# Performance work log

Hardware: AMD Instinct MI355X
Metric: run time of the kernel (lower is better)

The kernel has to match this reference:

```python
import jax, jax.numpy as jnp
import numpy as np

D = 1024   # dim == seq_len L (forced by final proj on [L, L])
N = 16     # SSM state size
K = 3      # conv kernel size, padding=1 -> same length


def setup_inputs() -> dict:
    key = jax.random.key(0)
    ks = jax.random.split(key, 8)
    s = lambda k, shape, sc: (jax.random.normal(k, shape, jnp.float32) * sc)
    return {
        "x": s(ks[0], (2, D, D), 1.0),
        "W_proj": s(ks[1], (D, D), D ** -0.5),
        "b_proj": jnp.zeros((D,), jnp.float32),
        "conv_w": s(ks[2], (D, D, K), (D * K) ** -0.5),  # [out_ch, in_ch, K]
        "conv_b": jnp.zeros((D,), jnp.float32),
        "A_log": jnp.log(jnp.tile(jnp.arange(1, N + 1, dtype=jnp.float32)[None, :], (D, 1))),  # [D, N]
        "W_delta": s(ks[3], (D, D), D ** -0.5),
        "W_B": s(ks[4], (D, N), D ** -0.5),
        "W_C": s(ks[5], (D, N), D ** -0.5),
    }


def _ssm(x, A_log, W_delta, W_B, W_C):
    # Mamba S6 diagonal selective scan. x: [L, D]
    delta = jax.nn.softplus(x @ W_delta)            # [L, D]
    B = x @ W_B                                      # [L, N]
    C = x @ W_C                                      # [L, N]
    A = -jnp.exp(A_log)                              # [D, N]
    Abar = jnp.exp(delta[:, :, None] * A[None])      # [L, D, N]
    Bx = (delta * x)[:, :, None] * B[:, None, :]     # [L, D, N]

    def combine(e1, e2):
        a1, b1 = e1
        a2, b2 = e2
        return a1 * a2, a2 * b1 + b2

    _, h = jax.lax.associative_scan(combine, (Abar, Bx), axis=0)  # h: [L, D, N]
    return jnp.einsum('ldn,ln->ld', h, C)            # [L, D]


def reference(x, W_proj, b_proj, conv_w, conv_b, A_log, W_delta, W_B, W_C):
    p = x @ W_proj.T + b_proj                        # shared proj; [2, L, D]
    xm, xg = p[0], p[1]                              # mirrors `x, x_ = self.proj(x)` unpacking batch==2
    xg = jax.nn.silu(xg)                             # [L, D]
    # Conv1d treats xm as (channels=L, length=D), padding=1 -> same length
    xc = jax.lax.conv_general_dilated(
        xm[None], conv_w, window_strides=(1,), padding=[(1, 1)],
        dimension_numbers=('NCW', 'OIW', 'NCW'))[0] + conv_b[:, None]  # [L, D]
    xc = jax.nn.silu(xc)
    y = _ssm(xc, A_log, W_delta, W_B, W_C)           # [L, D]
    y = y @ xg.T                                     # [L, L]  (x @ x_.transpose(-1,-2))
    return y @ W_proj.T + b_proj                     # final shared proj; [L, L]
```

## Files before the change

### kernel.cpp

```cpp
#include <hip/hip_runtime.h>
#include <math.h>


#define LL 1024
#define DD 1024
#define NS 16
#define CCH 16
#define CLEN 64

typedef short     bf16x8_t __attribute__((ext_vector_type(8)));
typedef float     f32x4_t  __attribute__((ext_vector_type(4)));
typedef unsigned short u16x4_t __attribute__((ext_vector_type(4)));
typedef unsigned short u16x8_t __attribute__((ext_vector_type(8)));

__device__ __forceinline__ float silu_f(float x) { return x / (1.f + expf(-x)); }
__device__ __forceinline__ float softplus_f(float x) {
  return fmaxf(x, 0.f) + log1pf(expf(-fabsf(x)));
}
__device__ __forceinline__ unsigned short f2bf(float f) {
  unsigned int u = __float_as_uint(f);
  u += 0x7fffu + ((u >> 16) & 1u);
  return (unsigned short)(u >> 16);
}

template<int N> __device__ __forceinline__ void s_wait_vmcnt() {
  asm volatile("s_waitcnt vmcnt(%0)" :: "n"(N) : "memory");
}
__device__ __forceinline__ void raw_barrier() {
  asm volatile("s_barrier" ::: "memory");
}

__global__ __launch_bounds__(256) void castk(const float* __restrict__ in,
                                             unsigned short* __restrict__ out, int n) {
  int i = (blockIdx.x * 256 + threadIdx.x) * 4;
  if (i >= n) return;
  float4 v = *(const float4*)(in + i);
  u16x4_t o; o[0] = f2bf(v.x); o[1] = f2bf(v.y); o[2] = f2bf(v.z); o[3] = f2bf(v.w);
  *(u16x4_t*)(out + i) = o;
}

__global__ __launch_bounds__(256) void tcastk(const float* __restrict__ W,
                                              unsigned short* __restrict__ out) {
  __shared__ float T[64][65];
  const int t = threadIdx.x;
  const int r = t >> 2, cq = (t & 3) << 4;
  const int d0 = blockIdx.x * 64, k0 = blockIdx.y * 64;
  #pragma unroll
  for (int c = 0; c < 16; c += 4) {
    float4 v = *(const float4*)&W[(size_t)(k0 + r) * DD + d0 + cq + c];
    T[r][cq + c + 0] = v.x; T[r][cq + c + 1] = v.y;
    T[r][cq + c + 2] = v.z; T[r][cq + c + 3] = v.w;
  }
  __syncthreads();
  u16x8_t o0, o1;
  #pragma unroll
  for (int j = 0; j < 8; ++j) o0[j] = f2bf(T[cq + j][r]);
  #pragma unroll
  for (int j = 0; j < 8; ++j) o1[j] = f2bf(T[cq + 8 + j][r]);
  *(u16x8_t*)&out[(size_t)(d0 + r) * DD + k0 + cq] = o0;
  *(u16x8_t*)&out[(size_t)(d0 + r) * DD + k0 + cq + 8] = o1;
}

__global__ __launch_bounds__(256) void bct_cast(const float* __restrict__ WB,
                                                const float* __restrict__ WC,
                                                unsigned short* __restrict__ wcomb) {
  const int b = blockIdx.x;
  const int k = threadIdx.x * 4;
  u16x4_t o;
  if (b < 32) {
    const float* W = (b < 16) ? WB : WC;
    const int n = b & 15;
    #pragma unroll
    for (int j = 0; j < 4; ++j) o[j] = f2bf(W[(size_t)(k + j) * NS + n]);
  } else {
    o[0] = o[1] = o[2] = o[3] = 0;
  }
  *(u16x4_t*)&wcomb[(size_t)(1024 + b) * DD + k] = o;
}

__global__ __launch_bounds__(256) void build_xsht(const unsigned short* __restrict__ xm,
                                                  unsigned short* __restrict__ out) {
  __shared__ unsigned short Xs[64][66];
  const int t = threadIdx.x;
  const int w0 = blockIdx.x * 64, i0 = blockIdx.y * 64;
  {
    const int r = t >> 2, cq = (t & 3) << 4;
    #pragma unroll
    for (int c = 0; c < 16; c += 4) {
      u16x4_t v = *(const u16x4_t*)&xm[(size_t)(i0 + r) * DD + w0 + cq + c];
      Xs[r][1 + cq + c + 0] = v[0]; Xs[r][1 + cq + c + 1] = v[1];
      Xs[r][1 + cq + c + 2] = v[2]; Xs[r][1 + cq + c + 3] = v[3];
    }
  }
  if (t < 64)                 Xs[t][0]       = (w0 > 0)        ? xm[(size_t)(i0 + t) * DD + w0 - 1]  : (unsigned short)0;
  else if (t < 128) { int r = t - 64; Xs[r][65] = (w0 + 64 < DD) ? xm[(size_t)(i0 + r) * DD + w0 + 64] : (unsigned short)0; }
  __syncthreads();
  const int wr = t >> 2, q = t & 3;
  unsigned short vals[48];
  #pragma unroll
  for (int ii = 0; ii < 16; ++ii)
    #pragma unroll
    for (int k = 0; k < 3; ++k)
      vals[ii * 3 + k] = Xs[q * 16 + ii][wr + k];
  #pragma unroll
  for (int s = 0; s < 6; ++s) {
    u16x8_t o;
    #pragma unroll
    for (int j = 0; j < 8; ++j) o[j] = vals[s * 8 + j];
    *(u16x8_t*)&out[(size_t)(w0 + wr) * 3072 + (size_t)i0 * 3 + q * 48 + s * 8] = o;
  }
}

__global__ __launch_bounds__(256) void gemm_sk(
    const unsigned short* __restrict__ A, const unsigned short* __restrict__ B,
    float* __restrict__ part, size_t sliceStride, int N, int K, int Ksl)
{
  constexpr int GI = 4;
  __shared__ unsigned short s[3][256 * 32];
  const int tid  = threadIdx.x;
  const int lane = tid & 63;
  const int wv   = tid >> 6;
  const int wm   = wv >> 1, wn = wv & 1;
  const int m0 = blockIdx.y * 128, n0 = blockIdx.x * 128;
  const int wbase = tid & 192;
  const int koff = blockIdx.z * Ksl;

  f32x4_t acc[4][4];
  #pragma unroll
  for (int i = 0; i < 4; ++i)
    #pragma unroll
    for (int j = 0; j < 4; ++j)
      acc[i][j] = (f32x4_t)(0.f);

  auto stage = [&](int buf, int kbase) {
    #pragma unroll
    for (int it = 0; it < GI; ++it) {
      const int c   = (it << 8) + tid;
      const int r   = c >> 2;
      const int kcg = (c & 3) ^ ((r >> 1) & 3);
      const unsigned short* src = (r < 128)
          ? (A + (size_t)(m0 + r) * K + kbase + kcg * 8)
          : (B + (size_t)(n0 + r - 128) * K + kbase + kcg * 8);
      __builtin_amdgcn_global_load_lds(
          (const __attribute__((address_space(1))) void*)src,
          (__attribute__((address_space(3))) void*)(&s[buf][0] + (size_t)((it << 8) + wbase) * 8),
          16, 0, 0);
    }
  };

  const int NT = Ksl >> 5;
  stage(0, koff);
  stage(1, koff + 32);
  s_wait_vmcnt<GI>();
  raw_barrier();

  for (int t = 0; t < NT; ++t) {
    if (t + 2 < NT) stage((t + 2) % 3, koff + (t + 2) * 32);

    const unsigned short* sb = &s[t % 3][0];
    const int rl = lane & 15, kq = lane >> 4;
    bf16x8_t af[4], bfr[4];
    #pragma unroll
    for (int mi = 0; mi < 4; ++mi) {
      const int row = wm * 64 + mi * 16 + rl;
      const int ch  = row * 4 + (kq ^ ((row >> 1) & 3));
      af[mi] = *(const bf16x8_t*)(sb + (size_t)ch * 8);
    }
    #pragma unroll
    for (int ni = 0; ni < 4; ++ni) {
      const int row = 128 + wn * 64 + ni * 16 + rl;
      const int ch  = row * 4 + (kq ^ ((row >> 1) & 3));
      bfr[ni] = *(const bf16x8_t*)(sb + (size_t)ch * 8);
    }
    #pragma unroll
    for (int mi = 0; mi < 4; ++mi)
      #pragma unroll
      for (int ni = 0; ni < 4; ++ni)
        acc[mi][ni] = __builtin_amdgcn_mfma_f32_16x16x32_bf16(af[mi], bfr[ni], acc[mi][ni], 0, 0, 0);

    if (t + 1 < NT) {
      if (t + 2 < NT) s_wait_vmcnt<GI>();
      else            s_wait_vmcnt<0>();
      raw_barrier();
    }
  }

  float* pz = part + (size_t)blockIdx.z * sliceStride;
  const int rl = lane & 15, rg = lane >> 4;
  #pragma unroll
  for (int mi = 0; mi < 4; ++mi) {
    #pragma unroll
    for (int ni = 0; ni < 4; ++ni) {
      const int col = n0 + wn * 64 + ni * 16 + rl;
      #pragma unroll
      for (int j = 0; j < 4; ++j) {
        const int row = m0 + wm * 64 + mi * 16 + rg * 4 + j;
        pz[(size_t)row * N + col] = acc[mi][ni][j];
      }
    }
  }
}

template<int SK, int ACT, bool O32, bool O16>
__global__ __launch_bounds__(256) void reduce_k(
    const float* __restrict__ part, size_t sliceStride,
    const float* __restrict__ bias,
    float* __restrict__ C32, unsigned short* __restrict__ C16)
{
  const size_t idx = ((size_t)blockIdx.x * 256 + threadIdx.x) * 4;
  const int row = (int)(idx >> 10), col = (int)(idx & 1023);
  float4 s = *(const float4*)&part[idx];
  #pragma unroll
  for (int z = 1; z < SK; ++z) {
    const float4 p = *(const float4*)&part[(size_t)z * sliceStride + idx];
    s.x += p.x; s.y += p.y; s.z += p.z; s.w += p.w;
  }
  float v[4] = {s.x, s.y, s.z, s.w};
  if (bias) {
    const float4 bv = *(const float4*)&bias[col];
    v[0] += bv.x; v[1] += bv.y; v[2] += bv.z; v[3] += bv.w;
  }
  #pragma unroll
  for (int j = 0; j < 4; ++j) {
    if (ACT == 2) v[j] = softplus_f(v[j]);
    else if (ACT == 3) { if (row >= 1024) v[j] = silu_f(v[j]); }
    else if (ACT == 4) { if (row < 1024)  v[j] = softplus_f(v[j]); }
  }
  if (O32) { float4 o; o.x = v[0]; o.y = v[1]; o.z = v[2]; o.w = v[3];
             *(float4*)&C32[idx] = o; }
  if (O16) { u16x4_t o; o[0] = f2bf(v[0]); o[1] = f2bf(v[1]);
             o[2] = f2bf(v[2]); o[3] = f2bf(v[3]);
             *(u16x4_t*)&C16[idx] = o; }
}

__global__ __launch_bounds__(256) void reduce_conv_t(
    const float* __restrict__ part, const float* __restrict__ cb,
    unsigned short* __restrict__ xc16, float* __restrict__ xcT)
{
  __shared__ float T[64][65];
  const int t = threadIdx.x;
  const int r = t >> 4;
  const int cq = (t & 15) << 2;
  const int r0 = blockIdx.y * 64, c0 = blockIdx.x * 64;
  #pragma unroll
  for (int rr = 0; rr < 64; rr += 16) {
    const int row = r0 + r + rr;
    const size_t base = (size_t)row * 1024 + c0 + cq;
    float4 s = *(const float4*)&part[base];
    #pragma unroll
    for (int z = 1; z < 4; ++z) {
      const float4 p = *(const float4*)&part[(size_t)z * (1024 * 1024) + base];
      s.x += p.x; s.y += p.y; s.z += p.z; s.w += p.w;
    }
    const float b = cb[row];
    float v[4] = {silu_f(s.x + b), silu_f(s.y + b), silu_f(s.z + b), silu_f(s.w + b)};
    u16x4_t o16; o16[0] = f2bf(v[0]); o16[1] = f2bf(v[1]);
    o16[2] = f2bf(v[2]); o16[3] = f2bf(v[3]);
    *(u16x4_t*)&xc16[base] = o16;
    T[r + rr][cq + 0] = v[0]; T[r + rr][cq + 1] = v[1];
    T[r + rr][cq + 2] = v[2]; T[r + rr][cq + 3] = v[3];
  }
  __syncthreads();
  #pragma unroll
  for (int rr = 0; rr < 64; rr += 16) {
    float4 o;
    o.x = T[cq + 0][r + rr]; o.y = T[cq + 1][r + rr];
    o.z = T[cq + 2][r + rr]; o.w = T[cq + 3][r + rr];
    *(float4*)&xcT[(size_t)(c0 + r + rr) * LL + r0 + cq] = o;
  }
}

__global__ __launch_bounds__(256) void scan_p1(
    const float* __restrict__ deltaT, const float* __restrict__ xcT,
    const float* __restrict__ BT, const float* __restrict__ A_log,
    float* __restrict__ P, float* __restrict__ H)
{
  const int tid = threadIdx.x;
  const int n = tid & 15, dl = tid >> 4;
  const int d = blockIdx.y * 16 + dl;
  const int c = blockIdx.x;
  const int l0 = c * CLEN;
  const float Av = -expf(A_log[d * NS + n]);
  float h = 0.f, p = 1.f;
  for (int j = 0; j < CLEN; j += 4) {
    const float4 dv = *(const float4*)&deltaT[(size_t)d * LL + l0 + j];
    const float4 xv = *(const float4*)&xcT[(size_t)d * LL + l0 + j];
    const float4 bv = *(const float4*)&BT[(size_t)n * LL + l0 + j];
    const float dvu[4] = {dv.x, dv.y, dv.z, dv.w};
    const float xvu[4] = {xv.x, xv.y, xv.z, xv.w};
    const float bvu[4] = {bv.x, bv.y, bv.z, bv.w};
    #pragma unroll
    for (int u = 0; u < 4; ++u) {
      const float ab = expf(dvu[u] * Av);
      h = fmaf(ab, h, dvu[u] * xvu[u] * bvu[u]);
      p *= ab;
    }
  }
  const int idx = d * NS + n;
  P[(size_t)c * (DD * NS) + idx] = p;
  H[(size_t)c * (DD * NS) + idx] = h;
}

__global__ __launch_bounds__(256) void scan_p2(const float* __restrict__ P,
                                               const float* __restrict__ H,
                                               float* __restrict__ Hin) {
  const int idx = blockIdx.x * 256 + threadIdx.x;
  float hin = 0.f;
  Hin[idx] = 0.f;
  #pragma unroll
  for (int c = 1; c < CCH; ++c) {
    hin = fmaf(P[(size_t)(c - 1) * (DD * NS) + idx], hin,
               H[(size_t)(c - 1) * (DD * NS) + idx]);
    Hin[(size_t)c * (DD * NS) + idx] = hin;
  }
}

__global__ __launch_bounds__(256) void scan_p3(
    const float* __restrict__ deltaT, const float* __restrict__ xcT,
    const float* __restrict__ BT, const float* __restrict__ CT,
    const float* __restrict__ Hin, const float* __restrict__ A_log,
    unsigned short* __restrict__ y16)
{
  const int tid = threadIdx.x;
  const int n = tid & 15, dl = tid >> 4;
  const int d = blockIdx.y * 16 + dl;
  const int c = blockIdx.x;
  const int l0 = c * CLEN;
  const float Av = -expf(A_log[d * NS + n]);
  float h = Hin[(size_t)c * (DD * NS) + d * NS + n];
  for (int j = 0; j < CLEN; j += 4) {
    const float4 dv = *(const float4*)&deltaT[(size_t)d * LL + l0 + j];
    const float4 xv = *(const float4*)&xcT[(size_t)d * LL + l0 + j];
    const float4 bv = *(const float4*)&BT[(size_t)n * LL + l0 + j];
    const float4 cv = *(const float4*)&CT[(size_t)n * LL + l0 + j];
    const float dvu[4] = {dv.x, dv.y, dv.z, dv.w};
    const float xvu[4] = {xv.x, xv.y, xv.z, xv.w};
    const float bvu[4] = {bv.x, bv.y, bv.z, bv.w};
    const float cvu[4] = {cv.x, cv.y, cv.z, cv.w};
    #pragma unroll
    for (int u = 0; u < 4; ++u) {
      const int l = l0 + j + u;
      const float ab = expf(dvu[u] * Av);
      h = fmaf(ab, h, dvu[u] * xvu[u] * bvu[u]);
      float contrib = h * cvu[u];
      contrib += __shfl_xor(contrib, 1);
      contrib += __shfl_xor(contrib, 2);
      contrib += __shfl_xor(contrib, 4);
      contrib += __shfl_xor(contrib, 8);
      if (n == 0) y16[(size_t)l * DD + d] = f2bf(contrib);
    }
  }
}

extern "C" void kernel_launch(void* const* d_in, const int* in_sizes, int n_in,
                              void* d_out, int out_size, void* d_ws, size_t ws_size,
                              hipStream_t stream) {
  const float* x       = (const float*)d_in[0];
  const float* W_proj  = (const float*)d_in[1];
  const float* b_proj  = (const float*)d_in[2];
  const float* conv_w  = (const float*)d_in[3];
  const float* conv_b  = (const float*)d_in[4];
  const float* A_log   = (const float*)d_in[5];
  const float* W_delta = (const float*)d_in[6];
  const float* W_B     = (const float*)d_in[7];
  const float* W_C     = (const float*)d_in[8];
  float* out = (float*)d_out;

  char* w = (char*)d_ws;
  const size_t QMB = 256 * 1024;
  unsigned short* wp16    = (unsigned short*)(w);
  unsigned short* pbuf    = (unsigned short*)(w + 8  * QMB);
  unsigned short* xm16    = pbuf;
  unsigned short* xg16    = pbuf + 1024 * 1024;
  unsigned short* wcomb16 = (unsigned short*)(w + 24 * QMB);
  unsigned short* xc16    = (unsigned short*)(w + 34 * QMB);
  float*          xcT32   = (float*)(w + 42 * QMB);
  unsigned short* x16     = (unsigned short*)(w + 58 * QMB);
  float*          dcomb32 = (float*)(w + 58 * QMB);
  float*          deltaT32= dcomb32;
  float*          BT32    = dcomb32 + (size_t)1024 * 1024;
  float*          CT32    = dcomb32 + (size_t)1040 * 1024;
  unsigned short* cw16    = (unsigned short*)(w + 75 * QMB);
  unsigned short* y16     = (unsigned short*)(w + 75 * QMB);
  float*          Pc      = (float*)(w + 83 * QMB);
  float*          Hc      = (float*)(w + 87 * QMB);
  float*          HinC    = (float*)(w + 91 * QMB);
  unsigned short* out116  = (unsigned short*)(w + 87 * QMB);
  unsigned short* xsht    = (unsigned short*)(w + 99 * QMB);
  float*          part    = (float*)(w + 123 * QMB);
  (void)ws_size;

  const dim3 blk(256);

  castk<<<dim3(2048), blk, 0, stream>>>(x, x16, 2 * 1024 * 1024);
  castk<<<dim3(1024), blk, 0, stream>>>(W_proj, wp16, 1024 * 1024);
  castk<<<dim3(3072), blk, 0, stream>>>(conv_w, cw16, 3 * 1024 * 1024);
  tcastk<<<dim3(16, 16), blk, 0, stream>>>(W_delta, wcomb16);
  bct_cast<<<dim3(128), blk, 0, stream>>>(W_B, W_C, wcomb16);

  gemm_sk<<<dim3(8, 16, 2), blk, 0, stream>>>(x16, wp16, part,
      (size_t)2048 * 1024, 1024, 1024, 512);
  reduce_k<2, 3, false, true><<<dim3(2048), blk, 0, stream>>>(
      part, (size_t)2048 * 1024, b_proj, nullptr, pbuf);
  build_xsht<<<dim3(16, 16), blk, 0, stream>>>(xm16, xsht);
  gemm_sk<<<dim3(8, 8, 4), blk, 0, stream>>>(cw16, xsht, part,
      (size_t)1024 * 1024, 1024, 3072, 768);
  reduce_conv_t<<<dim3(16, 16), blk, 0, stream>>>(part, conv_b, xc16, xcT32);
  gemm_sk<<<dim3(8, 9, 2), blk, 0, stream>>>(wcomb16, xc16, part,
      (size_t)1152 * 1024, 1024, 1024, 512);
  reduce_k<2, 4, true, false><<<dim3(1056), blk, 0, stream>>>(
      part, (size_t)1152 * 1024, nullptr, dcomb32, nullptr);
  scan_p1<<<dim3(CCH, DD / 16), blk, 0, stream>>>(deltaT32, xcT32, BT32, A_log, Pc, Hc);
  scan_p2<<<dim3(64), blk, 0, stream>>>(Pc, Hc, HinC);
  scan_p3<<<dim3(CCH, DD / 16), blk, 0, stream>>>(deltaT32, xcT32, BT32, CT32, HinC, A_log, y16);
  gemm_sk<<<dim3(8, 8, 4), blk, 0, stream>>>(y16, xg16, part,
      (size_t)1024 * 1024, 1024, 1024, 256);
  reduce_k<4, 0, false, true><<<dim3(1024), blk, 0, stream>>>(
      part, (size_t)1024 * 1024, nullptr, nullptr, out116);
  gemm_sk<<<dim3(8, 8, 4), blk, 0, stream>>>(out116, wp16, part,
      (size_t)1024 * 1024, 1024, 1024, 256);
  reduce_k<4, 0, true, false><<<dim3(1024), blk, 0, stream>>>(
      part, (size_t)1024 * 1024, b_proj, out, nullptr);
}
```

Before: 225.2 us.

## Shrink GEMM tiles to 64x64 with BK=64, fuse epilogue, cut split-K

The GEMM kernel now uses 64x64 output tiles with a 64-wide K step and an 8-way XOR swizzle, in place of 128x128 tiles with a 32-wide K step. The first projection GEMM drops split-K and applies bias and SiLU in a fused epilogue, which removes one reduce kernel. The other GEMMs use split-K of 2 instead of 4 to cut partial-sum traffic, and the three cast kernels are merged into one launch. Smaller tiles give more blocks and better occupancy but lower per-block data reuse, and the fused epilogue writes scalar bf16 values without coalescing.

Result: faster. 203.3 us (-9.7%).

```diff
diff --git a/kernel.cpp b/kernel.cpp
--- a/kernel.cpp
+++ b/kernel.cpp
@@ -30,13 +30,18 @@
   asm volatile("s_barrier" ::: "memory");
 }
 
-__global__ __launch_bounds__(256) void castk(const float* __restrict__ in,
-                                             unsigned short* __restrict__ out, int n) {
-  int i = (blockIdx.x * 256 + threadIdx.x) * 4;
-  if (i >= n) return;
-  float4 v = *(const float4*)(in + i);
+__global__ __launch_bounds__(256) void cast_all(
+    const float* __restrict__ x, const float* __restrict__ wp,
+    const float* __restrict__ cw, unsigned short* __restrict__ x16,
+    unsigned short* __restrict__ wp16, unsigned short* __restrict__ cw16) {
+  const size_t i = ((size_t)blockIdx.x * 256 + threadIdx.x) * 4;
+  const float* in; unsigned short* out; size_t off;
+  if (i < 2097152)      { in = x;  out = x16;  off = 0; }
+  else if (i < 3145728) { in = wp; out = wp16; off = 2097152; }
+  else                  { in = cw; out = cw16; off = 3145728; }
+  const float4 v = *(const float4*)(in + (i - off));
   u16x4_t o; o[0] = f2bf(v.x); o[1] = f2bf(v.y); o[2] = f2bf(v.z); o[3] = f2bf(v.w);
-  *(u16x4_t*)(out + i) = o;
+  *(u16x4_t*)(out + (i - off)) = o;
 }
 
 __global__ __launch_bounds__(256) void tcastk(const float* __restrict__ W,
@@ -111,36 +116,39 @@
   }
 }
 
-__global__ __launch_bounds__(256) void gemm_sk(
+template<int ACT, bool BROW, bool O32, bool O16, bool PART>
+__global__ __launch_bounds__(256) void gemm_bf16(
     const unsigned short* __restrict__ A, const unsigned short* __restrict__ B,
-    float* __restrict__ part, size_t sliceStride, int N, int K, int Ksl)
+    const float* __restrict__ bias, float* __restrict__ C32,
+    unsigned short* __restrict__ C16, int M, int N, int K, int Ksl,
+    size_t sliceStride)
 {
   constexpr int GI = 4;
-  __shared__ unsigned short s[3][256 * 32];
+  __shared__ unsigned short s[3][128 * 64];
   const int tid  = threadIdx.x;
   const int lane = tid & 63;
   const int wv   = tid >> 6;
   const int wm   = wv >> 1, wn = wv & 1;
-  const int m0 = blockIdx.y * 128, n0 = blockIdx.x * 128;
+  const int m0 = blockIdx.y * 64, n0 = blockIdx.x * 64;
   const int wbase = tid & 192;
-  const int koff = blockIdx.z * Ksl;
-
-  f32x4_t acc[4][4];
-  #pragma unroll
-  for (int i = 0; i < 4; ++i)
-    #pragma unroll
-    for (int j = 0; j < 4; ++j)
+  const int koff = PART ? blockIdx.z * Ksl : 0;
+
+  f32x4_t acc[2][2];
+  #pragma unroll
+  for (int i = 0; i < 2; ++i)
+    #pragma unroll
+    for (int j = 0; j < 2; ++j)
       acc[i][j] = (f32x4_t)(0.f);
 
   auto stage = [&](int buf, int kbase) {
     #pragma unroll
     for (int it = 0; it < GI; ++it) {
       const int c   = (it << 8) + tid;
-      const int r   = c >> 2;
-      const int kcg = (c & 3) ^ ((r >> 1) & 3);
-      const unsigned short* src = (r < 128)
+      const int r   = c >> 3;
+      const int kcg = (c & 7) ^ (r & 7);
+      const unsigned short* src = (r < 64)
           ? (A + (size_t)(m0 + r) * K + kbase + kcg * 8)
-          : (B + (size_t)(n0 + r - 128) * K + kbase + kcg * 8);
+          : (B + (size_t)(n0 + r - 64) * K + kbase + kcg * 8);
       __builtin_amdgcn_global_load_lds(
           (const __attribute__((address_space(1))) void*)src,
           (__attribute__((address_space(3))) void*)(&s[buf][0] + (size_t)((it << 8) + wbase) * 8),
@@ -148,35 +156,44 @@
     }
   };
 
-  const int NT = Ksl >> 5;
+  const int NT = Ksl >> 6;
   stage(0, koff);
-  stage(1, koff + 32);
+  stage(1, koff + 64);
   s_wait_vmcnt<GI>();
   raw_barrier();
 
   for (int t = 0; t < NT; ++t) {
-    if (t + 2 < NT) stage((t + 2) % 3, koff + (t + 2) * 32);
+    if (t + 2 < NT) stage((t + 2) % 3, koff + (t + 2) * 64);
 
     const unsigned short* sb = &s[t % 3][0];
     const int rl = lane & 15, kq = lane >> 4;
-    bf16x8_t af[4], bfr[4];
-    #pragma unroll
-    for (int mi = 0; mi < 4; ++mi) {
-      const int row = wm * 64 + mi * 16 + rl;
-      const int ch  = row * 4 + (kq ^ ((row >> 1) & 3));
-      af[mi] = *(const bf16x8_t*)(sb + (size_t)ch * 8);
-    }
-    #pragma unroll
-    for (int ni = 0; ni < 4; ++ni) {
-      const int row = 128 + wn * 64 + ni * 16 + rl;
-      const int ch  = row * 4 + (kq ^ ((row >> 1) & 3));
-      bfr[ni] = *(const bf16x8_t*)(sb + (size_t)ch * 8);
-    }
-    #pragma unroll
-    for (int mi = 0; mi < 4; ++mi)
+    bf16x8_t af[2][2], bfr[2][2];
+    #pragma unroll
+    for (int mi = 0; mi < 2; ++mi) {
+      const int row = wm * 32 + mi * 16 + rl;
       #pragma unroll
-      for (int ni = 0; ni < 4; ++ni)
-        acc[mi][ni] = __builtin_amdgcn_mfma_f32_16x16x32_bf16(af[mi], bfr[ni], acc[mi][ni], 0, 0, 0);
+      for (int ks = 0; ks < 2; ++ks) {
+        const int ch = row * 8 + ((ks * 4 + kq) ^ (row & 7));
+        af[mi][ks] = *(const bf16x8_t*)(sb + (size_t)ch * 8);
+      }
+    }
+    #pragma unroll
+    for (int ni = 0; ni < 2; ++ni) {
+      const int row = 64 + wn * 32 + ni * 16 + rl;
+      #pragma unroll
+      for (int ks = 0; ks < 2; ++ks) {
+        const int ch = row * 8 + ((ks * 4 + kq) ^ (row & 7));
+        bfr[ni][ks] = *(const bf16x8_t*)(sb + (size_t)ch * 8);
+      }
+    }
+    #pragma unroll
+    for (int mi = 0; mi < 2; ++mi)
+      #pragma unroll
+      for (int ni = 0; ni < 2; ++ni)
+        #pragma unroll
+        for (int ks = 0; ks < 2; ++ks)
+          acc[mi][ni] = __builtin_amdgcn_mfma_f32_16x16x32_bf16(
+              af[mi][ks], bfr[ni][ks], acc[mi][ni], 0, 0, 0);
 
     if (t + 1 < NT) {
       if (t + 2 < NT) s_wait_vmcnt<GI>();
@@ -185,17 +202,28 @@
     }
   }
 
-  float* pz = part + (size_t)blockIdx.z * sliceStride;
   const int rl = lane & 15, rg = lane >> 4;
-  #pragma unroll
-  for (int mi = 0; mi < 4; ++mi) {
-    #pragma unroll
-    for (int ni = 0; ni < 4; ++ni) {
-      const int col = n0 + wn * 64 + ni * 16 + rl;
+  float* outp = PART ? (C32 + (size_t)blockIdx.z * sliceStride) : C32;
+  #pragma unroll
+  for (int mi = 0; mi < 2; ++mi) {
+    #pragma unroll
+    for (int ni = 0; ni < 2; ++ni) {
+      const int col = n0 + wn * 32 + ni * 16 + rl;
       #pragma unroll
       for (int j = 0; j < 4; ++j) {
-        const int row = m0 + wm * 64 + mi * 16 + rg * 4 + j;
-        pz[(size_t)row * N + col] = acc[mi][ni][j];
+        const int row = m0 + wm * 32 + mi * 16 + rg * 4 + j;
+        float v = acc[mi][ni][j];
+        if (PART) {
+          outp[(size_t)row * N + col] = v;
+        } else {
+          if (bias) v += BROW ? bias[row] : bias[col];
+          if (ACT == 1) v = silu_f(v);
+          else if (ACT == 2) v = softplus_f(v);
+          else if (ACT == 3) { if (row >= 1024) v = silu_f(v); }
+          else if (ACT == 4) { if (row < 1024)  v = softplus_f(v); }
+          if (O32) C32[(size_t)row * N + col] = v;
+          if (O16) C16[(size_t)row * N + col] = f2bf(v);
+        }
       }
     }
   }
@@ -223,8 +251,7 @@
   #pragma unroll
   for (int j = 0; j < 4; ++j) {
     if (ACT == 2) v[j] = softplus_f(v[j]);
-    else if (ACT == 3) { if (row >= 1024) v[j] = silu_f(v[j]); }
-    else if (ACT == 4) { if (row < 1024)  v[j] = softplus_f(v[j]); }
+    else if (ACT == 4) { if (row < 1024) v[j] = softplus_f(v[j]); }
   }
   if (O32) { float4 o; o.x = v[0]; o.y = v[1]; o.z = v[2]; o.w = v[3];
              *(float4*)&C32[idx] = o; }
@@ -233,6 +260,7 @@
              *(u16x4_t*)&C16[idx] = o; }
 }
 
+template<int SK>
 __global__ __launch_bounds__(256) void reduce_conv_t(
     const float* __restrict__ part, const float* __restrict__ cb,
     unsigned short* __restrict__ xc16, float* __restrict__ xcT)
@@ -248,7 +276,7 @@
     const size_t base = (size_t)row * 1024 + c0 + cq;
     float4 s = *(const float4*)&part[base];
     #pragma unroll
-    for (int z = 1; z < 4; ++z) {
+    for (int z = 1; z < SK; ++z) {
       const float4 p = *(const float4*)&part[(size_t)z * (1024 * 1024) + base];
       s.x += p.x; s.y += p.y; s.z += p.z; s.w += p.w;
     }
@@ -392,33 +420,33 @@
 
   const dim3 blk(256);
 
-  castk<<<dim3(2048), blk, 0, stream>>>(x, x16, 2 * 1024 * 1024);
-  castk<<<dim3(1024), blk, 0, stream>>>(W_proj, wp16, 1024 * 1024);
-  castk<<<dim3(3072), blk, 0, stream>>>(conv_w, cw16, 3 * 1024 * 1024);
+  cast_all<<<dim3(6144), blk, 0, stream>>>(x, W_proj, conv_w, x16, wp16, cw16);
   tcastk<<<dim3(16, 16), blk, 0, stream>>>(W_delta, wcomb16);
   bct_cast<<<dim3(128), blk, 0, stream>>>(W_B, W_C, wcomb16);
 
-  gemm_sk<<<dim3(8, 16, 2), blk, 0, stream>>>(x16, wp16, part,
-      (size_t)2048 * 1024, 1024, 1024, 512);
-  reduce_k<2, 3, false, true><<<dim3(2048), blk, 0, stream>>>(
-      part, (size_t)2048 * 1024, b_proj, nullptr, pbuf);
+  gemm_bf16<3, false, false, true, false><<<dim3(16, 32), blk, 0, stream>>>(
+      x16, wp16, b_proj, nullptr, pbuf, 2048, 1024, 1024, 1024, 0);
   build_xsht<<<dim3(16, 16), blk, 0, stream>>>(xm16, xsht);
-  gemm_sk<<<dim3(8, 8, 4), blk, 0, stream>>>(cw16, xsht, part,
-      (size_t)1024 * 1024, 1024, 3072, 768);
-  reduce_conv_t<<<dim3(16, 16), blk, 0, stream>>>(part, conv_b, xc16, xcT32);
-  gemm_sk<<<dim3(8, 9, 2), blk, 0, stream>>>(wcomb16, xc16, part,
-      (size_t)1152 * 1024, 1024, 1024, 512);
+  gemm_bf16<0, false, true, false, true><<<dim3(16, 16, 2), blk, 0, stream>>>(
+      cw16, xsht, nullptr, part, nullptr, 1024, 1024, 3072, 1536,
+      (size_t)1024 * 1024);
+  reduce_conv_t<2><<<dim3(16, 16), blk, 0, stream>>>(part, conv_b, xc16, xcT32);
+  gemm_bf16<0, false, true, false, true><<<dim3(16, 18, 2), blk, 0, stream>>>(
+      wcomb16, xc16, nullptr, part, nullptr, 1152, 1024, 1024, 512,
+      (size_t)1152 * 1024);
   reduce_k<2, 4, true, false><<<dim3(1056), blk, 0, stream>>>(
       part, (size_t)1152 * 1024, nullptr, dcomb32, nullptr);
   scan_p1<<<dim3(CCH, DD / 16), blk, 0, stream>>>(deltaT32, xcT32, BT32, A_log, Pc, Hc);
   scan_p2<<<dim3(64), blk, 0, stream>>>(Pc, Hc, HinC);
   scan_p3<<<dim3(CCH, DD / 16), blk, 0, stream>>>(deltaT32, xcT32, BT32, CT32, HinC, A_log, y16);
-  gemm_sk<<<dim3(8, 8, 4), blk, 0, stream>>>(y16, xg16, part,
-      (size_t)1024 * 1024, 1024, 1024, 256);
-  reduce_k<4, 0, false, true><<<dim3(1024), blk, 0, stream>>>(
+  gemm_bf16<0, false, true, false, true><<<dim3(16, 16, 2), blk, 0, stream>>>(
+      y16, xg16, nullptr, part, nullptr, 1024, 1024, 1024, 512,
+      (size_t)1024 * 1024);
+  reduce_k<2, 0, false, true><<<dim3(1024), blk, 0, stream>>>(
       part, (size_t)1024 * 1024, nullptr, nullptr, out116);
-  gemm_sk<<<dim3(8, 8, 4), blk, 0, stream>>>(out116, wp16, part,
-      (size_t)1024 * 1024, 1024, 1024, 256);
-  reduce_k<4, 0, true, false><<<dim3(1024), blk, 0, stream>>>(
+  gemm_bf16<0, false, true, false, true><<<dim3(16, 16, 2), blk, 0, stream>>>(
+      out116, wp16, nullptr, part, nullptr, 1024, 1024, 1024, 512,
+      (size_t)1024 * 1024);
+  reduce_k<2, 0, true, false><<<dim3(1024), blk, 0, stream>>>(
       part, (size_t)1024 * 1024, b_proj, out, nullptr);
 }
```
